# Optimization experiments

Measured on AMD Instinct MI355X. Metric: run time of the kernel, lower is better.

Reference implementation:

```python
import jax, jax.numpy as jnp
import numpy as np

EMBED_DIM = 1280
NUM_HEADS = 32
HEAD_DIM = EMBED_DIM // NUM_HEADS  # 40
SCALING = HEAD_DIM ** -0.5
BSZ, TGT_LEN, PAST_LEN = 2, 1024, 1024


def setup_inputs() -> dict:
    key = jax.random.key(0)
    ks = jax.random.split(key, 8)
    w_scale = 1.0 / np.sqrt(EMBED_DIM)
    return {
        "inputs": jax.random.normal(ks[0], (BSZ, TGT_LEN, EMBED_DIM), jnp.float32),
        "past_key": jax.random.normal(ks[1], (BSZ, NUM_HEADS, PAST_LEN, HEAD_DIM), jnp.float32),
        "past_value": jax.random.normal(ks[2], (BSZ, NUM_HEADS, PAST_LEN, HEAD_DIM), jnp.float32),
        "Wq": jax.random.normal(ks[3], (EMBED_DIM, EMBED_DIM), jnp.float32) * w_scale,
        "bq": jnp.zeros((EMBED_DIM,), jnp.float32),
        "Wk": jax.random.normal(ks[4], (EMBED_DIM, EMBED_DIM), jnp.float32) * w_scale,
        "bk": jnp.zeros((EMBED_DIM,), jnp.float32),
        "Wv": jax.random.normal(ks[5], (EMBED_DIM, EMBED_DIM), jnp.float32) * w_scale,
        "bv": jnp.zeros((EMBED_DIM,), jnp.float32),
        "Wo": jax.random.normal(ks[6], (EMBED_DIM, EMBED_DIM), jnp.float32) * w_scale,
        "bo": jnp.zeros((EMBED_DIM,), jnp.float32),
    }


def _shape(x, bsz):
    # [b, s, e] -> [b, h, s, d]
    return x.reshape(bsz, -1, NUM_HEADS, HEAD_DIM).transpose(0, 2, 1, 3)


def reference(inputs, past_key, past_value, Wq, bq, Wk, bk, Wv, bv, Wo, bo):
    bsz, tgt_len, _ = inputs.shape
    # projections (dropout rate is 0 -> identity)
    q = _shape((inputs @ Wq + bq) * SCALING, bsz)        # [b,h,t,d]
    k_new = _shape(inputs @ Wk + bk, bsz)                # [b,h,t,d]
    v_new = _shape(inputs @ Wv + bv, bsz)
    # KV-cache concat along seq axis
    key_states = jnp.concatenate([past_key, k_new], axis=2)    # [b,h,s,d]
    value_states = jnp.concatenate([past_value, v_new], axis=2)
    # attention: QK^T -> softmax -> AV (full score matrix, as original)
    attn_weights = jnp.einsum('bhid,bhjd->bhij', q, key_states)  # [b,h,t,s]
    attn_probs = jax.nn.softmax(attn_weights, axis=-1)
    attn_output = jnp.einsum('bhij,bhjd->bhid', attn_probs, value_states)  # [b,h,t,d]
    attn_output = attn_output.transpose(0, 2, 1, 3).reshape(bsz, tgt_len, EMBED_DIM)
    attn_output = attn_output @ Wo + bo
    return attn_output, key_states, value_states
```

## Files before the change

### kernel.cpp

```cpp
#include <hip/hip_runtime.h>
#include <hip/hip_bf16.h>

#define ED 1280
#define NH 32
#define HD 40
#define BSZ 2
#define TL 1024
#define SEQ 2048
#define SCALING 0.15811388300841897f

typedef __bf16 bf16x8 __attribute__((ext_vector_type(8)));
typedef float floatx4 __attribute__((ext_vector_type(4)));
typedef unsigned short ushort;
typedef ushort ushortx8 __attribute__((ext_vector_type(8)));

__device__ __forceinline__ ushort f2bf(float f) {
    __hip_bfloat16 h = __float2bfloat16(f);
    return *(ushort*)&h;
}
__device__ __forceinline__ unsigned pk2(float a, float b) {
    return (unsigned)f2bf(a) | ((unsigned)f2bf(b) << 16);
}

#define ASYNC16(g, l)                                                                 \
    __builtin_amdgcn_global_load_lds((const __attribute__((address_space(1))) void*)(g), \
                                     (__attribute__((address_space(3))) void*)(l), 16, 0, 0)

__global__ void convert_x_zero(const float* X, ushort* Xb, ushort* Qb) {
    int bid = blockIdx.x;
    if (bid < 2560) {
        int i = (bid * 256 + threadIdx.x) * 4;
        float4 v = *(const float4*)&X[i];
        ushort4 o;
        o.x = f2bf(v.x); o.y = f2bf(v.y); o.z = f2bf(v.z); o.w = f2bf(v.w);
        *(ushort4*)&Xb[i] = o;
    } else {
        int i = ((bid - 2560) * 256 + threadIdx.x) * 8;
        uint4 z = {0, 0, 0, 0};
        *(uint4*)&Qb[i] = z;
    }
}

__global__ void transpose_w(const float* w0, const float* w1,
                            const float* w2, const float* w3, ushort* wt) {
    __shared__ float tile[32][33];
    int z = blockIdx.z;
    const float* w = (z == 0) ? w0 : (z == 1) ? w1 : (z == 2) ? w2 : w3;
    ushort* o = wt + (size_t)z * ED * ED;
    int n0 = blockIdx.x * 32, k0 = blockIdx.y * 32;
    int tx = threadIdx.x, ty = threadIdx.y;
#pragma unroll
    for (int i = ty; i < 32; i += 8) tile[i][tx] = w[(k0 + i) * ED + n0 + tx];
    __syncthreads();
#pragma unroll
    for (int i = ty; i < 32; i += 8) o[(n0 + i) * ED + k0 + tx] = f2bf(tile[tx][i]);
}

__global__ void copy_past(const float* PK, const float* PV, float* keyOut, float* valOut) {
    int idx = blockIdx.x * 256 + threadIdx.x;
    int which = idx >= 655360;
    int f4 = which ? idx - 655360 : idx;
    const float4* src = (const float4*)(which ? PV : PK);
    float4* dst = (float4*)(which ? valOut : keyOut);
    int bhj = f4 / 10, c4 = f4 - bhj * 10;
    int bh = bhj >> 10, j = bhj & 1023;
    dst[(bh * SEQ + j) * 10 + c4] = src[f4];
}

__global__ void prep_k(const float* keyOut, ushort* Kb16) {
    int idx = blockIdx.x * 256 + threadIdx.x;
    int row = idx / 6, j = idx - row * 6;
    uint4 o = {0, 0, 0, 0};
    if (j < 5) {
        const float* s = &keyOut[(size_t)row * 40 + j * 8];
        float4 a = *(const float4*)s;
        float4 b = *(const float4*)(s + 4);
        o.x = pk2(a.x, a.y); o.y = pk2(a.z, a.w);
        o.z = pk2(b.x, b.y); o.w = pk2(b.z, b.w);
    }
    *(uint4*)&Kb16[(size_t)row * 48 + j * 8] = o;
}

__global__ void prep_v(const float* valOut, ushort* Vt16) {
    __shared__ ushort T[48 * 72];
    int bh = blockIdx.x, st = blockIdx.y;
    int tid = threadIdx.x;
    for (int i = tid; i < 8 * 72; i += 256) {
        int dr = i / 72, k = i - dr * 72;
        T[(40 + dr) * 72 + k] = (dr == 0) ? 0x3F80 : 0;
    }
    const float* src = valOut + ((size_t)bh * SEQ + st * 64) * 40;
    for (int i = tid; i < 640; i += 256) {
        int key = i / 10, c = i - key * 10;
        float4 v = *(const float4*)&src[key * 40 + c * 4];
        T[(c * 4 + 0) * 72 + key] = f2bf(v.x);
        T[(c * 4 + 1) * 72 + key] = f2bf(v.y);
        T[(c * 4 + 2) * 72 + key] = f2bf(v.z);
        T[(c * 4 + 3) * 72 + key] = f2bf(v.w);
    }
    __syncthreads();
    ushort* dst = Vt16 + (size_t)bh * 48 * 2048 + st * 64;
    for (int i = tid; i < 384; i += 256) {
        int d = i >> 3, c = i & 7;
        *(uint4*)&dst[(size_t)d * 2048 + c * 8] = *(const uint4*)&T[d * 72 + c * 8];
    }
}

__device__ __forceinline__ void gemm_core(const ushort* A, const ushort* Bt,
                                          ushort* As, ushort* Bs,
                                          int m0, int n0, floatx4 acc[4][4]) {
    int tidx = threadIdx.x;
    int wave = tidx >> 6, lane = tidx & 63;
    int wm = (wave >> 1) * 64, wn = (wave & 1) * 64;
    int fr = lane & 15, kq = lane >> 4;
    for (int k0 = 0; k0 < ED; k0 += 32) {
#pragma unroll
        for (int p = 0; p < 2; ++p) {
            int flat = p * 2048 + tidx * 8;
            int r = flat >> 5, c = flat & 31;
            ASYNC16(&A[(m0 + r) * ED + k0 + c], &As[flat]);
            ASYNC16(&Bt[(n0 + r) * ED + k0 + c], &Bs[flat]);
        }
        __syncthreads();
        bf16x8 a[4], b[4];
#pragma unroll
        for (int mi = 0; mi < 4; ++mi) a[mi] = *(const bf16x8*)&As[(wm + mi * 16 + fr) * 32 + kq * 8];
#pragma unroll
        for (int ni = 0; ni < 4; ++ni) b[ni] = *(const bf16x8*)&Bs[(wn + ni * 16 + fr) * 32 + kq * 8];
#pragma unroll
        for (int mi = 0; mi < 4; ++mi)
#pragma unroll
            for (int ni = 0; ni < 4; ++ni)
                acc[mi][ni] = __builtin_amdgcn_mfma_f32_16x16x32_bf16(a[mi], b[ni], acc[mi][ni], 0, 0, 0);
        __syncthreads();
    }
}

__global__ __launch_bounds__(256) void gemm_qkv(const ushort* Xb, const ushort* Wt,
                                                const float* bq, const float* bk,
                                                const float* bv, ushort* Qb,
                                                float* keyOut, float* valOut) {
    __shared__ ushort As[128 * 32], Bs[128 * 32];
    int z = blockIdx.z;
    const ushort* Bt = Wt + (size_t)z * ED * ED;
    const float* bias = (z == 0) ? bq : (z == 1) ? bk : bv;
    int m0 = blockIdx.y * 128, n0 = blockIdx.x * 128;
    floatx4 acc[4][4] = {};
    gemm_core(Xb, Bt, As, Bs, m0, n0, acc);
    int lane = threadIdx.x & 63, wave = threadIdx.x >> 6;
    int wm = (wave >> 1) * 64, wn = (wave & 1) * 64;
    int cq = lane >> 4, cc = lane & 15;
#pragma unroll
    for (int mi = 0; mi < 4; ++mi)
#pragma unroll
        for (int ni = 0; ni < 4; ++ni) {
            int col = n0 + wn + ni * 16 + cc;
            float bvf = bias[col];
            int h = col / HD, dh = col - h * HD;
#pragma unroll
            for (int r = 0; r < 4; ++r) {
                int row = m0 + wm + mi * 16 + cq * 4 + r;
                int b = row >> 10, t = row & 1023;
                float v = acc[mi][ni][r] + bvf;
                if (z == 0) {
                    Qb[(((b * NH + h) * TL) + t) * 64 + dh] = f2bf(v * SCALING);
                } else {
                    int idx = ((b * NH + h) * SEQ + TL + t) * HD + dh;
                    (z == 1 ? keyOut : valOut)[idx] = v;
                }
            }
        }
}

__global__ __launch_bounds__(256) void gemm_out(const ushort* A, const ushort* Bt,
                                                const float* bias, float* out) {
    __shared__ ushort As[128 * 32], Bs[64 * 32];
    int m0 = blockIdx.y * 128, n0 = blockIdx.x * 64;
    int tidx = threadIdx.x;
    int wave = tidx >> 6, lane = tidx & 63;
    int wm = (wave >> 1) * 64, wn = (wave & 1) * 32;
    int fr = lane & 15, kq = lane >> 4;
    floatx4 acc[4][2] = {};
    for (int k0 = 0; k0 < ED; k0 += 32) {
#pragma unroll
        for (int p = 0; p < 2; ++p) {
            int flat = p * 2048 + tidx * 8;
            int r = flat >> 5, c = flat & 31;
            ASYNC16(&A[(m0 + r) * ED + k0 + c], &As[flat]);
        }
        {
            int flat = tidx * 8;
            int r = flat >> 5, c = flat & 31;
            ASYNC16(&Bt[(n0 + r) * ED + k0 + c], &Bs[flat]);
        }
        __syncthreads();
        bf16x8 a[4], b[2];
#pragma unroll
        for (int mi = 0; mi < 4; ++mi) a[mi] = *(const bf16x8*)&As[(wm + mi * 16 + fr) * 32 + kq * 8];
#pragma unroll
        for (int ni = 0; ni < 2; ++ni) b[ni] = *(const bf16x8*)&Bs[(wn + ni * 16 + fr) * 32 + kq * 8];
#pragma unroll
        for (int mi = 0; mi < 4; ++mi)
#pragma unroll
            for (int ni = 0; ni < 2; ++ni)
                acc[mi][ni] = __builtin_amdgcn_mfma_f32_16x16x32_bf16(a[mi], b[ni], acc[mi][ni], 0, 0, 0);
        __syncthreads();
    }
    int cq = lane >> 4, cc = lane & 15;
#pragma unroll
    for (int mi = 0; mi < 4; ++mi)
#pragma unroll
        for (int ni = 0; ni < 2; ++ni) {
            int col = n0 + wn + ni * 16 + cc;
            float bvf = bias[col];
#pragma unroll
            for (int r = 0; r < 4; ++r) {
                int row = m0 + wm + mi * 16 + cq * 4 + r;
                out[row * ED + col] = acc[mi][ni][r] + bvf;
            }
        }
}

__global__ __launch_bounds__(256) void attn_mfma(const ushort* Qb, const ushort* Kb16,
                                                 const ushort* Vt16, ushort* O) {
    __shared__ ushort Ks[2 * 128 * 64];
    __shared__ ushort Vs[2 * 48 * 128];

    int bh = blockIdx.x, b = bh >> 5, h = bh & 31;
    int tid = threadIdx.x, wave = tid >> 6, lane = tid & 63;
    int col = lane & 15, quad = lane >> 4;
    int qbase = blockIdx.y * 64 + wave * 16;

    bf16x8 qa[2];
#pragma unroll
    for (int ks = 0; ks < 2; ++ks)
        qa[ks] = *(const bf16x8*)(Qb + ((size_t)bh * TL + qbase + col) * 64 + ks * 32 + quad * 8);

    const ushort* ksrc[4];
    int kinc[4];
#pragma unroll
    for (int u = 0; u < 4; ++u) {
        int j = u * 256 + tid;
        int srow = j >> 3, ci = j & 7;
        int dch = ci ^ (srow & 7);
        int key = 32 * (srow >> 5) + 8 * ((srow >> 2) & 3) + 4 * ((srow >> 4) & 1) + (srow & 3);
        bool data = dch < 6;
        ksrc[u] = data ? Kb16 + ((size_t)bh * SEQ + key) * 48 + dch * 8 : Qb + 48;
        kinc[u] = data ? 128 * 48 : 0;
    }
    const ushort* vsrc[3];
#pragma unroll
    for (int u = 0; u < 3; ++u) {
        int j = u * 256 + tid;
        int row = j >> 4, ci = j & 15;
        int dch = (ci & 8) | ((ci & 7) ^ (row & 7));
        vsrc[u] = Vt16 + (size_t)bh * 48 * SEQ + (size_t)row * SEQ + dch * 8;
    }

    floatx4 Oacc[3] = {};
    int kxor = (col & 7) << 3;

#pragma unroll
    for (int u = 0; u < 4; ++u) {
        ASYNC16(ksrc[u], &Ks[(u * 256 + tid) * 8]);
        ksrc[u] += kinc[u];
    }
#pragma unroll
    for (int u = 0; u < 3; ++u) {
        ASYNC16(vsrc[u], &Vs[(u * 256 + tid) * 8]);
        vsrc[u] += 128;
    }
    __syncthreads();

#pragma unroll 1
    for (int t = 0; t < SEQ / 128; ++t) {
        ushort* KsC = Ks + (t & 1) * (128 * 64);
        ushort* VsC = Vs + (t & 1) * (48 * 128);
        if (t + 1 < SEQ / 128) {
            ushort* KsN = Ks + ((t + 1) & 1) * (128 * 64);
            ushort* VsN = Vs + ((t + 1) & 1) * (48 * 128);
#pragma unroll
            for (int u = 0; u < 4; ++u) {
                ASYNC16(ksrc[u], &KsN[(u * 256 + tid) * 8]);
                ksrc[u] += kinc[u];
            }
#pragma unroll
            for (int u = 0; u < 3; ++u) {
                ASYNC16(vsrc[u], &VsN[(u * 256 + tid) * 8]);
                vsrc[u] += 128;
            }
        }

        __builtin_amdgcn_s_setprio(1);
        floatx4 S[8] = {};
#pragma unroll
        for (int ks = 0; ks < 2; ++ks)
#pragma unroll
            for (int n = 0; n < 8; ++n) {
                int row = n * 16 + col;
                bf16x8 kb = *(const bf16x8*)&KsC[row * 64 + (((ks * 4 + quad) << 3) ^ kxor)];
                S[n] = __builtin_amdgcn_mfma_f32_16x16x32_bf16(kb, qa[ks], S[n], 0, 0, 0);
            }

#pragma unroll
        for (int ks = 0; ks < 4; ++ks) {
            unsigned w[4];
#pragma unroll
            for (int pi = 0; pi < 4; ++pi) {
                int i0 = pi * 2, i1 = i0 + 1;
                float s0 = S[2 * ks + (i0 >> 2)][i0 & 3];
                float s1 = S[2 * ks + (i1 >> 2)][i1 & 3];
                unsigned b0 = (unsigned)(int)fmaf(s0, 184.6649652f, 14035.0f);
                unsigned b1 = (unsigned)(int)fmaf(s1, 184.6649652f, 14035.0f);
                w[pi] = b0 | (b1 << 16);
            }
            uint4 pw;
            pw.x = w[0]; pw.y = w[1]; pw.z = w[2]; pw.w = w[3];
            bf16x8 pa = __builtin_bit_cast(bf16x8, pw);
            int c = ks * 4 + quad;
            int cpos = (c & 8) * 8 + ((((c & 7) << 3) ^ kxor));
#pragma unroll
            for (int no = 0; no < 3; ++no) {
                int row = no * 16 + col;
                bf16x8 vb = *(const bf16x8*)&VsC[row * 128 + cpos];
                Oacc[no] = __builtin_amdgcn_mfma_f32_16x16x32_bf16(pa, vb, Oacc[no], 0, 0, 0);
            }
        }
        __builtin_amdgcn_s_setprio(0);

        __syncthreads();
    }

    float linv[4];
#pragma unroll
    for (int r = 0; r < 4; ++r)
        linv[r] = 1.f / __shfl(Oacc[2][r], (lane & 48) + 8, 64);
#pragma unroll
    for (int n = 0; n < 3; ++n) {
        int d = n * 16 + col;
        if (d < HD) {
#pragma unroll
            for (int r = 0; r < 4; ++r) {
                int q = qbase + quad * 4 + r;
                O[(size_t)(b * TL + q) * ED + h * HD + d] = f2bf(Oacc[n][r] * linv[r]);
            }
        }
    }
}

extern "C" void kernel_launch(void* const* d_in, const int* in_sizes, int n_in,
                              void* d_out, int out_size, void* d_ws, size_t ws_size,
                              hipStream_t stream) {
    const float* X  = (const float*)d_in[0];
    const float* PK = (const float*)d_in[1];
    const float* PV = (const float*)d_in[2];
    const float* Wq = (const float*)d_in[3];
    const float* bq = (const float*)d_in[4];
    const float* Wk = (const float*)d_in[5];
    const float* bk = (const float*)d_in[6];
    const float* Wv = (const float*)d_in[7];
    const float* bv = (const float*)d_in[8];
    const float* Wo = (const float*)d_in[9];
    const float* bo = (const float*)d_in[10];

    float* out = (float*)d_out;
    float* keyOut = out + 2621440;
    float* valOut = keyOut + 5242880;

    ushort* ws   = (ushort*)d_ws;
    ushort* Wt   = ws;
    ushort* Qb   = Wt + 4 * (ED * ED);
    ushort* Kb16 = Qb + (size_t)65536 * 64;
    ushort* Vt16 = Kb16 + (size_t)131072 * 48;
    ushort* Xb   = Vt16 + (size_t)64 * 48 * 2048;
    ushort* Aws  = Xb;

    convert_x_zero<<<dim3(4608), dim3(256), 0, stream>>>(X, Xb, Qb);
    transpose_w<<<dim3(40, 40, 4), dim3(32, 8), 0, stream>>>(Wq, Wk, Wv, Wo, Wt);
    copy_past<<<dim3(5120), dim3(256), 0, stream>>>(PK, PV, keyOut, valOut);
    gemm_qkv<<<dim3(10, 16, 3), dim3(256), 0, stream>>>(Xb, Wt, bq, bk, bv, Qb, keyOut, valOut);
    prep_k<<<dim3(3072), dim3(256), 0, stream>>>(keyOut, Kb16);
    prep_v<<<dim3(64, 32), dim3(256), 0, stream>>>(valOut, Vt16);
    attn_mfma<<<dim3(64, 16), dim3(256), 0, stream>>>(Qb, Kb16, Vt16, Aws);
    gemm_out<<<dim3(20, 16), dim3(256), 0, stream>>>(Aws, Wt + 3 * (ED * ED), bo, out);
}
```

Baseline: 250.5 us.

## Double-buffer shared-memory tiles in projection GEMMs and narrow QKV tile to 128x64

Replaces the single-buffered GEMM main loop with a double-buffered version that issues async global-to-LDS loads for the next K-slice while MFMAs run on the current one, leaving one barrier per iteration. The QKV projection GEMM moves from 128x128 to 128x64 output tiles, doubling its grid to 960 blocks so more of the GPU's compute units are busy, and the output projection now shares the same core. This trades more LDS per block and more redundant A-tile loads for better latency hiding and occupancy.

```diff
diff --git a/kernel.cpp b/kernel.cpp
--- a/kernel.cpp
+++ b/kernel.cpp
@@ -106,31 +106,40 @@
     }
 }
 
-__device__ __forceinline__ void gemm_core(const ushort* A, const ushort* Bt,
-                                          ushort* As, ushort* Bs,
-                                          int m0, int n0, floatx4 acc[4][4]) {
+__device__ __forceinline__ void gemm_core_db(const ushort* A, const ushort* Bt,
+                                             ushort* As, ushort* Bs,
+                                             int m0, int n0, floatx4 acc[4][2]) {
     int tidx = threadIdx.x;
     int wave = tidx >> 6, lane = tidx & 63;
-    int wm = (wave >> 1) * 64, wn = (wave & 1) * 64;
+    int wm = (wave >> 1) * 64, wn = (wave & 1) * 32;
     int fr = lane & 15, kq = lane >> 4;
+    int fa = tidx * 8, ra = fa >> 5, ca = fa & 31;
+    const ushort* a0 = &A[(m0 + ra) * ED + ca];
+    const ushort* a1 = &A[(m0 + 64 + ra) * ED + ca];
+    const ushort* bsrc = &Bt[(n0 + ra) * ED + ca];
+    ASYNC16(a0, &As[fa]);
+    ASYNC16(a1, &As[2048 + fa]);
+    ASYNC16(bsrc, &Bs[fa]);
+    __syncthreads();
     for (int k0 = 0; k0 < ED; k0 += 32) {
-#pragma unroll
-        for (int p = 0; p < 2; ++p) {
-            int flat = p * 2048 + tidx * 8;
-            int r = flat >> 5, c = flat & 31;
-            ASYNC16(&A[(m0 + r) * ED + k0 + c], &As[flat]);
-            ASYNC16(&Bt[(n0 + r) * ED + k0 + c], &Bs[flat]);
-        }
-        __syncthreads();
-        bf16x8 a[4], b[4];
-#pragma unroll
-        for (int mi = 0; mi < 4; ++mi) a[mi] = *(const bf16x8*)&As[(wm + mi * 16 + fr) * 32 + kq * 8];
-#pragma unroll
-        for (int ni = 0; ni < 4; ++ni) b[ni] = *(const bf16x8*)&Bs[(wn + ni * 16 + fr) * 32 + kq * 8];
+        int cur = (k0 >> 5) & 1;
+        if (k0 + 32 < ED) {
+            int nxt = cur ^ 1;
+            ASYNC16(a0 + k0 + 32, &As[nxt * 4096 + fa]);
+            ASYNC16(a1 + k0 + 32, &As[nxt * 4096 + 2048 + fa]);
+            ASYNC16(bsrc + k0 + 32, &Bs[nxt * 2048 + fa]);
+        }
+        bf16x8 a[4], b[2];
 #pragma unroll
         for (int mi = 0; mi < 4; ++mi)
-#pragma unroll
-            for (int ni = 0; ni < 4; ++ni)
+            a[mi] = *(const bf16x8*)&As[cur * 4096 + (wm + mi * 16 + fr) * 32 + kq * 8];
+#pragma unroll
+        for (int ni = 0; ni < 2; ++ni)
+            b[ni] = *(const bf16x8*)&Bs[cur * 2048 + (wn + ni * 16 + fr) * 32 + kq * 8];
+#pragma unroll
+        for (int mi = 0; mi < 4; ++mi)
+#pragma unroll
+            for (int ni = 0; ni < 2; ++ni)
                 acc[mi][ni] = __builtin_amdgcn_mfma_f32_16x16x32_bf16(a[mi], b[ni], acc[mi][ni], 0, 0, 0);
         __syncthreads();
     }
@@ -140,20 +149,20 @@
                                                 const float* bq, const float* bk,
                                                 const float* bv, ushort* Qb,
                                                 float* keyOut, float* valOut) {
-    __shared__ ushort As[128 * 32], Bs[128 * 32];
+    __shared__ ushort As[2 * 128 * 32], Bs[2 * 64 * 32];
     int z = blockIdx.z;
     const ushort* Bt = Wt + (size_t)z * ED * ED;
     const float* bias = (z == 0) ? bq : (z == 1) ? bk : bv;
-    int m0 = blockIdx.y * 128, n0 = blockIdx.x * 128;
-    floatx4 acc[4][4] = {};
-    gemm_core(Xb, Bt, As, Bs, m0, n0, acc);
+    int m0 = blockIdx.y * 128, n0 = blockIdx.x * 64;
+    floatx4 acc[4][2] = {};
+    gemm_core_db(Xb, Bt, As, Bs, m0, n0, acc);
     int lane = threadIdx.x & 63, wave = threadIdx.x >> 6;
-    int wm = (wave >> 1) * 64, wn = (wave & 1) * 64;
+    int wm = (wave >> 1) * 64, wn = (wave & 1) * 32;
     int cq = lane >> 4, cc = lane & 15;
 #pragma unroll
     for (int mi = 0; mi < 4; ++mi)
 #pragma unroll
-        for (int ni = 0; ni < 4; ++ni) {
+        for (int ni = 0; ni < 2; ++ni) {
             int col = n0 + wn + ni * 16 + cc;
             float bvf = bias[col];
             int h = col / HD, dh = col - h * HD;
@@ -174,38 +183,12 @@
 
 __global__ __launch_bounds__(256) void gemm_out(const ushort* A, const ushort* Bt,
                                                 const float* bias, float* out) {
-    __shared__ ushort As[128 * 32], Bs[64 * 32];
+    __shared__ ushort As[2 * 128 * 32], Bs[2 * 64 * 32];
     int m0 = blockIdx.y * 128, n0 = blockIdx.x * 64;
-    int tidx = threadIdx.x;
-    int wave = tidx >> 6, lane = tidx & 63;
+    floatx4 acc[4][2] = {};
+    gemm_core_db(A, Bt, As, Bs, m0, n0, acc);
+    int lane = threadIdx.x & 63, wave = threadIdx.x >> 6;
     int wm = (wave >> 1) * 64, wn = (wave & 1) * 32;
-    int fr = lane & 15, kq = lane >> 4;
-    floatx4 acc[4][2] = {};
-    for (int k0 = 0; k0 < ED; k0 += 32) {
-#pragma unroll
-        for (int p = 0; p < 2; ++p) {
-            int flat = p * 2048 + tidx * 8;
-            int r = flat >> 5, c = flat & 31;
-            ASYNC16(&A[(m0 + r) * ED + k0 + c], &As[flat]);
-        }
-        {
-            int flat = tidx * 8;
-            int r = flat >> 5, c = flat & 31;
-            ASYNC16(&Bt[(n0 + r) * ED + k0 + c], &Bs[flat]);
-        }
-        __syncthreads();
-        bf16x8 a[4], b[2];
-#pragma unroll
-        for (int mi = 0; mi < 4; ++mi) a[mi] = *(const bf16x8*)&As[(wm + mi * 16 + fr) * 32 + kq * 8];
-#pragma unroll
-        for (int ni = 0; ni < 2; ++ni) b[ni] = *(const bf16x8*)&Bs[(wn + ni * 16 + fr) * 32 + kq * 8];
-#pragma unroll
-        for (int mi = 0; mi < 4; ++mi)
-#pragma unroll
-            for (int ni = 0; ni < 2; ++ni)
-                acc[mi][ni] = __builtin_amdgcn_mfma_f32_16x16x32_bf16(a[mi], b[ni], acc[mi][ni], 0, 0, 0);
-        __syncthreads();
-    }
     int cq = lane >> 4, cc = lane & 15;
 #pragma unroll
     for (int mi = 0; mi < 4; ++mi)
@@ -378,7 +361,7 @@
     convert_x_zero<<<dim3(4608), dim3(256), 0, stream>>>(X, Xb, Qb);
     transpose_w<<<dim3(40, 40, 4), dim3(32, 8), 0, stream>>>(Wq, Wk, Wv, Wo, Wt);
     copy_past<<<dim3(5120), dim3(256), 0, stream>>>(PK, PV, keyOut, valOut);
-    gemm_qkv<<<dim3(10, 16, 3), dim3(256), 0, stream>>>(Xb, Wt, bq, bk, bv, Qb, keyOut, valOut);
+    gemm_qkv<<<dim3(20, 16, 3), dim3(256), 0, stream>>>(Xb, Wt, bq, bk, bv, Qb, keyOut, valOut);
     prep_k<<<dim3(3072), dim3(256), 0, stream>>>(keyOut, Kb16);
     prep_v<<<dim3(64, 32), dim3(256), 0, stream>>>(valOut, Vt16);
     attn_mfma<<<dim3(64, 16), dim3(256), 0, stream>>>(Qb, Kb16, Vt16, Aws);
```

Result: no change. 252.0 us (+0.6%).
